# Kernel optimization log

Hardware: AMD Instinct MI355X
Metric: run time of the kernel (lower is better)

The kernel has to match this reference:

```python
import jax, jax.numpy as jnp
import numpy as np

STATE_DIM = 128
HIDDEN = 128
NUM_HEADS = 16
TEMPERATURE = 1.0
NEG_INF = float('-inf')


def setup_inputs() -> dict:
    key = jax.random.key(0)
    ks = jax.random.split(key, 8)
    B, S = 2, 512
    state_embeddings = jax.random.normal(ks[0], (B, S, STATE_DIM), dtype=jnp.float32)
    mask = jnp.ones((B, S, S), dtype=bool)
    # MLP params (Linear stores [in, out] here; we apply x @ W + b)
    W1 = jax.random.normal(ks[1], (2 * STATE_DIM, HIDDEN), dtype=jnp.float32) / np.sqrt(2 * STATE_DIM)
    b1 = jnp.zeros((HIDDEN,), dtype=jnp.float32)
    W2 = jax.random.normal(ks[2], (HIDDEN, HIDDEN), dtype=jnp.float32) / np.sqrt(HIDDEN)
    b2 = jnp.zeros((HIDDEN,), dtype=jnp.float32)
    W3 = jax.random.normal(ks[3], (HIDDEN, NUM_HEADS), dtype=jnp.float32) / np.sqrt(HIDDEN)
    b3 = jnp.zeros((NUM_HEADS,), dtype=jnp.float32)
    head_temperatures = jnp.ones((NUM_HEADS,), dtype=jnp.float32) * TEMPERATURE
    return {
        'state_embeddings': state_embeddings,
        'mask': mask,
        'W1': W1, 'b1': b1, 'W2': W2, 'b2': b2, 'W3': W3, 'b3': b3,
        'head_temperatures': head_temperatures,
    }


def reference(state_embeddings, mask, W1, b1, W2, b2, W3, b3, head_temperatures):
    # Split first Linear: cat([x_i, x_j]) @ W1 == x_i @ W1a + x_j @ W1b
    # This avoids materializing the [B, S, S, 2*state_dim] pairwise concat
    # while computing identical math.
    W1a, W1b = W1[:STATE_DIM], W1[STATE_DIM:]
    hi = jnp.einsum('bsd,dh->bsh', state_embeddings, W1a) + b1  # [B,S,H]
    hj = jnp.einsum('bsd,dh->bsh', state_embeddings, W1b)       # [B,S,H]
    h = jax.nn.relu(hi[:, :, None, :] + hj[:, None, :, :])       # [B,S,S,H]
    h = jax.nn.relu(jnp.einsum('bijh,hk->bijk', h, W2) + b2)     # [B,S,S,H]
    comp = jnp.einsum('bijh,hn->bijn', h, W3) + b3               # [B,S,S,heads]
    bias = jnp.transpose(comp, (0, 3, 1, 2))                     # [B,heads,S,S]
    bias = bias * head_temperatures[None, :, None, None]
    bias = jnp.where(mask[:, None, :, :], bias, NEG_INF)
    return bias
```

## Files before the change

### kernel.cpp

```cpp
#include <hip/hip_runtime.h>
#include <math.h>

typedef _Float16 half8 __attribute__((ext_vector_type(8)));
typedef _Float16 half4v __attribute__((ext_vector_type(4)));
typedef float floatx4 __attribute__((ext_vector_type(4)));

__global__ __launch_bounds__(256) void prep_kernel(
    const float* __restrict__ E,
    const float* __restrict__ W1,
    const float* __restrict__ b1,
    const float* __restrict__ W2,
    const float* __restrict__ W3,
    _Float16* __restrict__ hih,
    _Float16* __restrict__ hjh,
    _Float16* __restrict__ W2frag,
    _Float16* __restrict__ W3frag)
{
    const int blk = blockIdx.x;
    const int t = threadIdx.x;
    if (blk < 256) {
        __shared__ float sE[4][128];
        const int r0 = blk * 4;
        for (int e = t; e < 512; e += 256)
            sE[e >> 7][e & 127] = E[r0*128 + e];
        __syncthreads();
        const int half = t >> 7;
        const int k = t & 127;
        float a0 = half ? 0.f : b1[k];
        float a1 = a0, a2 = a0, a3 = a0;
        const float* w1col = &W1[half*128*128 + k];
        #pragma unroll 8
        for (int d = 0; d < 128; ++d) {
            const float w = w1col[d*128];
            a0 = fmaf(sE[0][d], w, a0);
            a1 = fmaf(sE[1][d], w, a1);
            a2 = fmaf(sE[2][d], w, a2);
            a3 = fmaf(sE[3][d], w, a3);
        }
        _Float16* dst = half ? hjh : hih;
        dst[(r0+0)*128 + k] = (_Float16)a0;
        dst[(r0+1)*128 + k] = (_Float16)a1;
        dst[(r0+2)*128 + k] = (_Float16)a2;
        dst[(r0+3)*128 + k] = (_Float16)a3;
    } else if (blk == 256) {
        for (int e = t; e < 16384; e += 256) {
            int q = e & 7, l = (e >> 3) & 63, g = e >> 9;
            int wr = g >> 4, nt = (g >> 2) & 3, ks = g & 3;
            int row = 64*wr + 16*nt + (l & 15);
            int k = ks*32 + (l >> 4)*8 + q;
            W2frag[e] = (_Float16)W2[k*128 + row];
        }
    } else {
        for (int e = t; e < 2048; e += 256) {
            int q = e & 7, l = (e >> 3) & 63, ks = e >> 9;
            int k = ks*32 + (l >> 4)*8 + q;
            W3frag[e] = (_Float16)W3[k*16 + (l & 15)];
        }
    }
}

__device__ __forceinline__ int swz(int row, int chunk) {
    return row*128 + ((chunk ^ (row & 7)) << 3);
}

__global__ __launch_bounds__(256, 2) void main_kernel(
    const _Float16* __restrict__ hih,
    const _Float16* __restrict__ hjh,
    const _Float16* __restrict__ W2frag,
    const _Float16* __restrict__ W3frag,
    const float* __restrict__ b2,
    const float* __restrict__ b3,
    const float* __restrict__ temps,
    const int* __restrict__ mask,
    float* __restrict__ out)
{
    __shared__ __align__(16) _Float16 sHJ[128 * 128];
    __shared__ __align__(16) _Float16 sH2[128 * 128];

    const int tid = threadIdx.x;
    const int bid = blockIdx.x;
    const int b  = bid >> 8;
    const int i0 = ((bid >> 2) & 63) << 3;
    const int j0 = (bid & 3) << 7;

    const int lane = tid & 63;
    const int wave = tid >> 6;
    const int wr = wave >> 1;
    const int wc = wave & 1;
    const int lr = lane & 15;
    const int lq = lane >> 4;
    const int m0 = 32*wave;

    const half8 zero8 = {};
    const _Float16* hirow = &hih[(b*512 + i0)*128];
    const _Float16* hjbase = &hjh[(b*512 + j0)*128];
    const half8* w2v = (const half8*)W2frag;
    const half8* w3v = (const half8*)W3frag;

    half8 aW[4][4];
    #pragma unroll
    for (int nt = 0; nt < 4; ++nt)
        #pragma unroll
        for (int ks = 0; ks < 4; ++ks)
            aW[nt][ks] = w2v[((wr*4 + nt)*4 + ks)*64 + lane];

    half8 w3F[4];
    #pragma unroll
    for (int ks = 0; ks < 4; ++ks)
        w3F[ks] = w3v[ks*64 + lane];

    float4 bv[4];
    #pragma unroll
    for (int nt = 0; nt < 4; ++nt)
        bv[nt] = *(const float4*)&b2[64*wr + 16*nt + 4*lq];

    half8 hiF[4];
    #pragma unroll
    for (int ks = 0; ks < 4; ++ks)
        hiF[ks] = *(const half8*)&hirow[ks*32 + lq*8];

    const int n2 = lr;
    const float tempv = temps[n2];
    const float b3v = b3[n2];

    #pragma unroll
    for (int kk = 0; kk < 8; ++kk) {
        const int c = kk*256 + tid;
        const int row = c >> 4, col = c & 15;
        half8 v = *(const half8*)&hjbase[row*128 + col*8];
        *(half8*)&sHJ[swz(row, col)] = v;
    }
    __syncthreads();

    for (int ii = 0; ii < 8; ++ii) {
        const int i = i0 + ii;

        floatx4 acc[4][4] = {};
        #pragma unroll
        for (int ks = 0; ks < 4; ++ks) {
            half8 bF[4];
            #pragma unroll
            for (int mt = 0; mt < 4; ++mt) {
                const int m = 64*wc + 16*mt + lr;
                half8 hj8 = *(const half8*)&sHJ[swz(m, ks*4 + lq)];
                bF[mt] = __builtin_elementwise_max(hiF[ks] + hj8, zero8);
            }
            #pragma unroll
            for (int nt = 0; nt < 4; ++nt)
                #pragma unroll
                for (int mt = 0; mt < 4; ++mt)
                    acc[nt][mt] = __builtin_amdgcn_mfma_f32_16x16x32_f16(
                        aW[nt][ks], bF[mt], acc[nt][mt], 0, 0, 0);
        }

        {
            const _Float16* hin = &hirow[((ii < 7) ? (ii + 1) : ii)*128];
            #pragma unroll
            for (int ks = 0; ks < 4; ++ks)
                hiF[ks] = *(const half8*)&hin[ks*32 + lq*8];
        }

        #pragma unroll
        for (int nt = 0; nt < 4; ++nt) {
            const int nb = 64*wr + 16*nt + 4*lq;
            #pragma unroll
            for (int mt = 0; mt < 4; ++mt) {
                const int m = 64*wc + 16*mt + lr;
                floatx4 v = acc[nt][mt];
                half4v o;
                o[0] = (_Float16)fmaxf(v[0] + bv[nt].x, 0.f);
                o[1] = (_Float16)fmaxf(v[1] + bv[nt].y, 0.f);
                o[2] = (_Float16)fmaxf(v[2] + bv[nt].z, 0.f);
                o[3] = (_Float16)fmaxf(v[3] + bv[nt].w, 0.f);
                *(half4v*)&sH2[swz(m, nb >> 3) + (nb & 7)] = o;
            }
        }

        const int* mrow = &mask[(b*512 + i)*512];
        int4 mk0 = *(const int4*)&mrow[j0 + m0 + 4*lq];
        int4 mk1 = *(const int4*)&mrow[j0 + m0 + 16 + 4*lq];
        __syncthreads();

        floatx4 acc2[2] = {};
        #pragma unroll
        for (int ks = 0; ks < 4; ++ks) {
            half8 a0v = *(const half8*)&sH2[swz(m0 + lr, ks*4 + lq)];
            half8 a1v = *(const half8*)&sH2[swz(m0 + 16 + lr, ks*4 + lq)];
            acc2[0] = __builtin_amdgcn_mfma_f32_16x16x32_f16(a0v, w3F[ks], acc2[0], 0, 0, 0);
            acc2[1] = __builtin_amdgcn_mfma_f32_16x16x32_f16(a1v, w3F[ks], acc2[1], 0, 0, 0);
        }

        float* outp = &out[(((b*16 + n2)*512) + i)*512];
        {
            const int j = j0 + m0 + 4*lq;
            floatx4 v = acc2[0];
            floatx4 res;
            res[0] = mk0.x ? (v[0] + b3v)*tempv : -INFINITY;
            res[1] = mk0.y ? (v[1] + b3v)*tempv : -INFINITY;
            res[2] = mk0.z ? (v[2] + b3v)*tempv : -INFINITY;
            res[3] = mk0.w ? (v[3] + b3v)*tempv : -INFINITY;
            __builtin_nontemporal_store(res, (floatx4*)&outp[j]);
        }
        {
            const int j = j0 + m0 + 16 + 4*lq;
            floatx4 v = acc2[1];
            floatx4 res;
            res[0] = mk1.x ? (v[0] + b3v)*tempv : -INFINITY;
            res[1] = mk1.y ? (v[1] + b3v)*tempv : -INFINITY;
            res[2] = mk1.z ? (v[2] + b3v)*tempv : -INFINITY;
            res[3] = mk1.w ? (v[3] + b3v)*tempv : -INFINITY;
            __builtin_nontemporal_store(res, (floatx4*)&outp[j]);
        }

        if (ii < 7) __syncthreads();
    }
}

extern "C" void kernel_launch(void* const* d_in, const int* in_sizes, int n_in,
                              void* d_out, int out_size, void* d_ws, size_t ws_size,
                              hipStream_t stream)
{
    const float* E     = (const float*)d_in[0];
    const int* mask    = (const int*)d_in[1];
    const float* W1    = (const float*)d_in[2];
    const float* b1    = (const float*)d_in[3];
    const float* W2    = (const float*)d_in[4];
    const float* b2    = (const float*)d_in[5];
    const float* W3    = (const float*)d_in[6];
    const float* b3    = (const float*)d_in[7];
    const float* temps = (const float*)d_in[8];

    char* ws = (char*)d_ws;
    _Float16* hih = (_Float16*)ws;
    _Float16* hjh = (_Float16*)(ws + 262144);
    _Float16* W2f = (_Float16*)(ws + 524288);
    _Float16* W3f = W2f + 16384;

    prep_kernel<<<258, 256, 0, stream>>>(E, W1, b1, W2, W3, hih, hjh, W2f, W3f);
    main_kernel<<<512, 256, 0, stream>>>(hih, hjh, W2f, W3f, b2, b3, temps, mask,
                                         (float*)d_out);
}
```

Before: 110.5 us.

## Compute W3 projection from per-wave fragments with split-K partial reduction via LDS

Each wave now writes its layer-2 ReLU output into a private LDS fragment buffer already laid out as MFMA A operands, then runs the W3 projection over its own 64-wide hidden slice. Waves with wr==1 deposit partial sums into a double-buffered LDS array, and waves with wr==0 add them, apply the mask, bias and temperature, and store. This drops the shared swizzled H2 tile and one of the two block barriers per row, cutting barrier stalls and cross-wave LDS traffic. In exchange, LDS use grows (fragment plus partial buffers), which may limit occupancy, and half the waves sit idle during the output stores.

Measured after the change: 111.1 us (median of 2 runs). About the same (+0.5%).

```diff
diff --git a/kernel.cpp b/kernel.cpp
--- a/kernel.cpp
+++ b/kernel.cpp
@@ -75,7 +75,8 @@
     float* __restrict__ out)
 {
     __shared__ __align__(16) _Float16 sHJ[128 * 128];
-    __shared__ __align__(16) _Float16 sH2[128 * 128];
+    __shared__ __align__(16) _Float16 sFrag[4 * 4096];
+    __shared__ __align__(16) float    sPart[2][2048];
 
     const int tid = threadIdx.x;
     const int bid = blockIdx.x;
@@ -89,7 +90,6 @@
     const int wc = wave & 1;
     const int lr = lane & 15;
     const int lq = lane >> 4;
-    const int m0 = 32*wave;
 
     const half8 zero8 = {};
     const _Float16* hirow = &hih[(b*512 + i0)*128];
@@ -104,10 +104,8 @@
         for (int ks = 0; ks < 4; ++ks)
             aW[nt][ks] = w2v[((wr*4 + nt)*4 + ks)*64 + lane];
 
-    half8 w3F[4];
-    #pragma unroll
-    for (int ks = 0; ks < 4; ++ks)
-        w3F[ks] = w3v[ks*64 + lane];
+    half8 w3A = w3v[(2*wr + 0)*64 + lane];
+    half8 w3B = w3v[(2*wr + 1)*64 + lane];
 
     float4 bv[4];
     #pragma unroll
@@ -119,9 +117,13 @@
     for (int ks = 0; ks < 4; ++ks)
         hiF[ks] = *(const half8*)&hirow[ks*32 + lq*8];
 
-    const int n2 = lr;
-    const float tempv = temps[n2];
-    const float b3v = b3[n2];
+    const float tempv = temps[lr];
+    const float b3v = b3[lr];
+
+    _Float16* myfrag = &sFrag[wave*4096];
+    const int tl_lo = lr + 16*(lq >> 1);
+    const int tl_hi = tl_lo + 32;
+    const int foff = (lq & 1) * 4;
 
     #pragma unroll
     for (int kk = 0; kk < 8; ++kk) {
@@ -162,57 +164,57 @@
 
         #pragma unroll
         for (int nt = 0; nt < 4; ++nt) {
-            const int nb = 64*wr + 16*nt + 4*lq;
+            const int tl = (nt & 1) ? tl_hi : tl_lo;
             #pragma unroll
             for (int mt = 0; mt < 4; ++mt) {
-                const int m = 64*wc + 16*mt + lr;
                 floatx4 v = acc[nt][mt];
                 half4v o;
                 o[0] = (_Float16)fmaxf(v[0] + bv[nt].x, 0.f);
                 o[1] = (_Float16)fmaxf(v[1] + bv[nt].y, 0.f);
                 o[2] = (_Float16)fmaxf(v[2] + bv[nt].z, 0.f);
                 o[3] = (_Float16)fmaxf(v[3] + bv[nt].w, 0.f);
-                *(half4v*)&sH2[swz(m, nb >> 3) + (nb & 7)] = o;
+                *(half4v*)&myfrag[(mt*2 + (nt >> 1))*512 + tl*8 + foff] = o;
             }
         }
 
-        const int* mrow = &mask[(b*512 + i)*512];
-        int4 mk0 = *(const int4*)&mrow[j0 + m0 + 4*lq];
-        int4 mk1 = *(const int4*)&mrow[j0 + m0 + 16 + 4*lq];
+        floatx4 acc2[4] = {};
+        #pragma unroll
+        for (int mt = 0; mt < 4; ++mt) {
+            half8 a0 = *(const half8*)&myfrag[(mt*2 + 0)*512 + lane*8];
+            half8 a1 = *(const half8*)&myfrag[(mt*2 + 1)*512 + lane*8];
+            acc2[mt] = __builtin_amdgcn_mfma_f32_16x16x32_f16(a0, w3A, acc2[mt], 0, 0, 0);
+            acc2[mt] = __builtin_amdgcn_mfma_f32_16x16x32_f16(a1, w3B, acc2[mt], 0, 0, 0);
+        }
+
+        float* pp = sPart[ii & 1];
+        int4 mk[4];
+        if (wr == 1) {
+            #pragma unroll
+            for (int mt = 0; mt < 4; ++mt)
+                *(floatx4*)&pp[wc*1024 + mt*256 + lane*4] = acc2[mt];
+        } else {
+            const int* mrow = &mask[(b*512 + i)*512];
+            #pragma unroll
+            for (int mt = 0; mt < 4; ++mt)
+                mk[mt] = *(const int4*)&mrow[j0 + 64*wc + 16*mt + 4*lq];
+        }
         __syncthreads();
 
-        floatx4 acc2[2] = {};
-        #pragma unroll
-        for (int ks = 0; ks < 4; ++ks) {
-            half8 a0v = *(const half8*)&sH2[swz(m0 + lr, ks*4 + lq)];
-            half8 a1v = *(const half8*)&sH2[swz(m0 + 16 + lr, ks*4 + lq)];
-            acc2[0] = __builtin_amdgcn_mfma_f32_16x16x32_f16(a0v, w3F[ks], acc2[0], 0, 0, 0);
-            acc2[1] = __builtin_amdgcn_mfma_f32_16x16x32_f16(a1v, w3F[ks], acc2[1], 0, 0, 0);
-        }
-
-        float* outp = &out[(((b*16 + n2)*512) + i)*512];
-        {
-            const int j = j0 + m0 + 4*lq;
-            floatx4 v = acc2[0];
-            floatx4 res;
-            res[0] = mk0.x ? (v[0] + b3v)*tempv : -INFINITY;
-            res[1] = mk0.y ? (v[1] + b3v)*tempv : -INFINITY;
-            res[2] = mk0.z ? (v[2] + b3v)*tempv : -INFINITY;
-            res[3] = mk0.w ? (v[3] + b3v)*tempv : -INFINITY;
-            __builtin_nontemporal_store(res, (floatx4*)&outp[j]);
-        }
-        {
-            const int j = j0 + m0 + 16 + 4*lq;
-            floatx4 v = acc2[1];
-            floatx4 res;
-            res[0] = mk1.x ? (v[0] + b3v)*tempv : -INFINITY;
-            res[1] = mk1.y ? (v[1] + b3v)*tempv : -INFINITY;
-            res[2] = mk1.z ? (v[2] + b3v)*tempv : -INFINITY;
-            res[3] = mk1.w ? (v[3] + b3v)*tempv : -INFINITY;
-            __builtin_nontemporal_store(res, (floatx4*)&outp[j]);
-        }
-
-        if (ii < 7) __syncthreads();
+        if (wr == 0) {
+            float* outp = &out[(((b*16 + lr)*512) + i)*512];
+            #pragma unroll
+            for (int mt = 0; mt < 4; ++mt) {
+                floatx4 p = *(const floatx4*)&pp[wc*1024 + mt*256 + lane*4];
+                floatx4 v = acc2[mt] + p;
+                const int j = j0 + 64*wc + 16*mt + 4*lq;
+                floatx4 res;
+                res[0] = mk[mt].x ? (v[0] + b3v)*tempv : -INFINITY;
+                res[1] = mk[mt].y ? (v[1] + b3v)*tempv : -INFINITY;
+                res[2] = mk[mt].z ? (v[2] + b3v)*tempv : -INFINITY;
+                res[3] = mk[mt].w ? (v[3] + b3v)*tempv : -INFINITY;
+                __builtin_nontemporal_store(res, (floatx4*)&outp[j]);
+            }
+        }
     }
 }
 
```
